# Kernel optimization log

Measured on AMD Instinct MI355X. Metric: run time of the kernel, lower is better.

Reference implementation:

```python
import jax, jax.numpy as jnp
import numpy as np

B, C, H, W = 8, 512, 32, 32
N = H * W
FG_THRES, BG_THRES, TOPK = 0.7, 0.6, 12


def setup_inputs() -> dict:
    key = jax.random.key(0)
    k1, k2, k3 = jax.random.split(key, 3)
    feature_q = jax.random.normal(k1, (B, C, H, W), dtype=jnp.float32)
    support_feat = jax.random.normal(k2, (B, C, H, W), dtype=jnp.float32)
    support_mask = jax.random.randint(k3, (B, H, W), 0, 2).astype(jnp.int32)
    return {"feature_q": feature_q, "support_feat": support_feat, "support_mask": support_mask}


def _masked_avg_pool(feat, mask):
    # feat [B,C,H,W], mask [B,1,H,W]; interpolate to same size is identity
    return jnp.sum(feat * mask, axis=(2, 3)) / (jnp.sum(mask, axis=(2, 3)) + 1e-5)


def _cosine(a, b):
    # F.cosine_similarity along channel dim 1 (eps=1e-8), with broadcasting
    dot = jnp.sum(a * b, axis=1)
    na = jnp.sqrt(jnp.sum(a * a, axis=1))
    nb = jnp.sqrt(jnp.sum(b * b, axis=1))
    return dot / jnp.maximum(na * nb, 1e-8)


def _similarity(feature_q, fg_proto, bg_proto):
    sim_fg = _cosine(feature_q, fg_proto)
    sim_bg = _cosine(feature_q, bg_proto)
    return jnp.stack([sim_bg, sim_fg], axis=1) * 10.0  # [B,2,H,W]


def _select_weights(pred, thres):
    # pred [N] -> float {0,1} selection weights; threshold mask, topk-12 fallback
    m = pred > thres
    _, top_idx = jax.lax.top_k(pred, TOPK)
    tm = jnp.zeros_like(m).at[top_idx].set(True)
    return jnp.where(m.sum() > 0, m, tm).astype(pred.dtype)


def _ssp_single(cur_feat, pred_fg, pred_bg):
    # cur_feat [C,N]; masked formulation == torch's variable-length column select
    wf = _select_weights(pred_fg, FG_THRES)
    wb = _select_weights(pred_bg, BG_THRES)
    fg_proto = jnp.sum(cur_feat * wf, axis=-1) / wf.sum()  # [C]
    bg_proto = jnp.sum(cur_feat * wb, axis=-1) / wb.sum()
    cn = cur_feat / jnp.sqrt(jnp.sum(cur_feat * cur_feat, axis=0, keepdims=True))
    sim = (cn.T @ cn) * 2.0  # [N,N] cosine sim, scaled
    neg = jnp.asarray(-1e30, sim.dtype)
    fg_attn = jax.nn.softmax(jnp.where(wf[None, :] > 0, sim, neg), axis=-1)
    bg_attn = jax.nn.softmax(jnp.where(wb[None, :] > 0, sim, neg), axis=-1)
    fg_local = (fg_attn @ cur_feat.T).T  # [C,N]
    bg_local = (bg_attn @ cur_feat.T).T
    return fg_proto, bg_proto, fg_local, bg_local


def reference(feature_q, support_feat, support_mask):
    mask_f = (support_mask == 1).astype(feature_q.dtype)[:, None]  # [B,1,H,W]
    mask_b = (support_mask == 0).astype(feature_q.dtype)[:, None]
    FP = _masked_avg_pool(support_feat, mask_f)[:, :, None, None]  # [B,C,1,1]
    BP = _masked_avg_pool(support_feat, mask_b)[:, :, None, None]
    out_0 = _similarity(feature_q, FP, BP)  # [B,2,H,W]
    pred = jax.nn.softmax(out_0, axis=1).reshape(B, 2, N)
    cur = feature_q.reshape(B, C, N)
    fg_p, bg_p, fg_l, bg_l = jax.vmap(_ssp_single)(cur, pred[:, 1], pred[:, 0])
    SSFP = fg_p[:, :, None, None]
    SSBP = bg_p[:, :, None, None]
    ASBP = bg_l.reshape(B, C, H, W)
    FP_1 = FP * 0.5 + SSFP * 0.5
    BP_1 = SSBP * 0.3 + ASBP * 0.7
    out_1 = _similarity(feature_q, FP_1, BP_1)  # [B,2,H,W]
    return out_1
```

## Files before the change

### kernel.cpp

```cpp
#include <hip/hip_runtime.h>
#include <math.h>

#define Bsz 8
#define Cch 512
#define Npx 1024
#define TOPK 12
#define BN (Bsz * Npx)

typedef __attribute__((ext_vector_type(8))) short bf16x8;
typedef __attribute__((ext_vector_type(4))) float f32x4;

__device__ __forceinline__ unsigned short f2bf(float x) {
    unsigned u = __float_as_uint(x);
    u += 0x7FFF + ((u >> 16) & 1);
    return (unsigned short)(u >> 16);
}
__device__ __forceinline__ float bf2f(unsigned short h) {
    return __uint_as_float(((unsigned)h) << 16);
}

__device__ __forceinline__ float warp_sum64(float v) {
    for (int o = 32; o > 0; o >>= 1) v += __shfl_down(v, o);
    return v;
}
__device__ __forceinline__ float block_sum512(float v, float* s8) {
    v = warp_sum64(v);
    int lane = threadIdx.x & 63, w = threadIdx.x >> 6;
    __syncthreads();
    if (lane == 0) s8[w] = v;
    __syncthreads();
    float r = 0.f;
    #pragma unroll
    for (int k = 0; k < 8; k++) r += s8[k];
    return r;
}

__global__ void k_pool(const float* __restrict__ sf, const int* __restrict__ mask,
                       float* __restrict__ FPo, float* __restrict__ BPo) {
    __shared__ float s4a[4], s4b[4], s4c[4];
    int c = blockIdx.x, b = blockIdx.y, t = threadIdx.x;
    const float4* f4 = (const float4*)(sf + ((size_t)b * Cch + c) * Npx);
    const int4* m4 = (const int4*)(mask + (size_t)b * Npx);
    float4 v = f4[t];
    int4 m = m4[t];
    float sumf = (m.x == 1 ? v.x : 0.f) + (m.y == 1 ? v.y : 0.f)
               + (m.z == 1 ? v.z : 0.f) + (m.w == 1 ? v.w : 0.f);
    float tot = v.x + v.y + v.z + v.w;
    float cf = (float)((m.x == 1) + (m.y == 1) + (m.z == 1) + (m.w == 1));
    sumf = warp_sum64(sumf);
    tot  = warp_sum64(tot);
    cf   = warp_sum64(cf);
    int lane = t & 63, w = t >> 6;
    if (lane == 0) { s4a[w] = sumf; s4b[w] = tot; s4c[w] = cf; }
    __syncthreads();
    if (t == 0) {
        float sA = s4a[0] + s4a[1] + s4a[2] + s4a[3];
        float sB = s4b[0] + s4b[1] + s4b[2] + s4b[3];
        float sC = s4c[0] + s4c[1] + s4c[2] + s4c[3];
        FPo[b * Cch + c] = sA / (sC + 1e-5f);
        BPo[b * Cch + c] = (sB - sA) / ((1024.f - sC) + 1e-5f);
    }
}

__global__ void __launch_bounds__(512) k_predcast(const float* __restrict__ fq,
                       const float* __restrict__ FP, const float* __restrict__ BP,
                       float* __restrict__ dsim, float* __restrict__ invn,
                       unsigned short* __restrict__ Ft, float* __restrict__ accs) {
    __shared__ float sFP[Cch], sBP[Cch], s8[8];
    __shared__ float rdf[16][32], rdb[16][32], rqq[16][32];
    __shared__ unsigned short S[32][522];
    int b = blockIdx.y, t = threadIdx.x;
    int tx = t & 31, ty = t >> 5;
    int p0 = blockIdx.x * 32;
    int p = p0 + tx;
    if (t < 128) accs[(size_t)(t >> 5) * BN + b * Npx + p0 + (t & 31)] = 0.f;
    sFP[t] = FP[b * Cch + t];
    sBP[t] = BP[b * Cch + t];
    __syncthreads();
    float nf = sqrtf(block_sum512(sFP[t] * sFP[t], s8));
    float nb = sqrtf(block_sum512(sBP[t] * sBP[t], s8));
    const float* q = fq + (size_t)b * Cch * Npx + p;
    float df = 0.f, db = 0.f, qq = 0.f;
    int c0 = ty * 32;
    #pragma unroll 4
    for (int c = 0; c < 32; c += 2) {
        float v0 = q[(size_t)(c0 + c) * Npx];
        float v1 = q[(size_t)(c0 + c + 1) * Npx];
        df += v0 * sFP[c0 + c] + v1 * sFP[c0 + c + 1];
        db += v0 * sBP[c0 + c] + v1 * sBP[c0 + c + 1];
        qq += v0 * v0 + v1 * v1;
        unsigned pk = (unsigned)f2bf(v0) | ((unsigned)f2bf(v1) << 16);
        *(unsigned*)&S[tx][c0 + c] = pk;
    }
    rdf[ty][tx] = df; rdb[ty][tx] = db; rqq[ty][tx] = qq;
    __syncthreads();
    for (int s = 8; s > 0; s >>= 1) {
        if (ty < s) {
            rdf[ty][tx] += rdf[ty + s][tx];
            rdb[ty][tx] += rdb[ty + s][tx];
            rqq[ty][tx] += rqq[ty + s][tx];
        }
        __syncthreads();
    }
    if (ty == 0) {
        float nq = sqrtf(rqq[0][tx]);
        float simf = 10.f * rdf[0][tx] / fmaxf(nq * nf, 1e-8f);
        float simb = 10.f * rdb[0][tx] / fmaxf(nq * nb, 1e-8f);
        dsim[b * Npx + p] = simf - simb;
        invn[b * Npx + p] = 1.f / nq;
    }
    int w = t >> 6, lane = t & 63;
    unsigned short* FtB = Ft + (size_t)b * Npx * Cch;
    for (int pr = w; pr < 32; pr += 8) {
        unsigned* dst = (unsigned*)(FtB + (size_t)(p0 + pr) * Cch);
        #pragma unroll
        for (int it = 0; it < 4; it++) {
            int d = it * 64 + lane;
            dst[d] = *(const unsigned*)&S[pr][d * 2];
        }
    }
}

__global__ void __launch_bounds__(1024) k_selcompact(const float* __restrict__ dsim,
                        const float* __restrict__ invn,
                        const unsigned short* __restrict__ Ft,
                        const float* __restrict__ FP,
                        int* __restrict__ nsf, int* __restrict__ nsb,
                        int* __restrict__ jf, int* __restrict__ jb,
                        float* __restrict__ ivg,
                        float* __restrict__ fgp, float* __restrict__ bgp,
                        float* __restrict__ FP1, float* __restrict__ nfv) {
    __shared__ int wsum[16];
    __shared__ int sns;
    __shared__ float sProto[16][512];
    __shared__ float s16f[16];
    int b = blockIdx.y, t = threadIdx.x;
    int lane = t & 63, w = t >> 6;
    bool isf = (blockIdx.x == 0);
    float d = dsim[b * Npx + t];
    float key = isf ? d : -d;
    float thres = isf ? 0.8472979f : 0.4054651f;
    int flag = (key > thres) ? 1 : 0;
    int x = flag;
    #pragma unroll
    for (int o = 1; o < 64; o <<= 1) {
        int y = __shfl_up(x, o);
        if (lane >= o) x += y;
    }
    if (lane == 63) wsum[w] = x;
    __syncthreads();
    int base = 0, total = 0;
    #pragma unroll
    for (int k = 0; k < 16; k++) {
        int s = wsum[k];
        if (k < w) base += s;
        total += s;
    }
    int* jdst = (isf ? jf : jb) + b * Npx;
    if (total == 0) {
        __shared__ int   sc[Npx];
        __shared__ float v[Npx];
        __shared__ float rv[Npx];
        __shared__ int   ri[Npx];
        v[t] = key; flag = 0;
        __syncthreads();
        for (int k = 0; k < TOPK; k++) {
            rv[t] = v[t]; ri[t] = t;
            __syncthreads();
            for (int s = 512; s > 0; s >>= 1) {
                if (t < s) {
                    float a = rv[t], bb = rv[t + s];
                    int ia = ri[t], ib = ri[t + s];
                    if (bb > a || (bb == a && ib < ia)) { rv[t] = bb; ri[t] = ib; }
                }
                __syncthreads();
            }
            int win = ri[0];
            if (t == win) { flag = 1; v[t] = -INFINITY; }
            __syncthreads();
        }
        sc[t] = flag;
        __syncthreads();
        for (int off = 1; off < 1024; off <<= 1) {
            int xx = (t >= off) ? sc[t - off] : 0;
            __syncthreads();
            sc[t] += xx;
            __syncthreads();
        }
        if (flag) {
            int pos = sc[t] - 1;
            jdst[pos] = t;
            if (!isf) ivg[b * Npx + pos] = invn[b * Npx + t];
        }
        if (t == 1023) sns = sc[1023];
    } else {
        if (flag) {
            int pos = base + x - 1;
            jdst[pos] = t;
            if (!isf) ivg[b * Npx + pos] = invn[b * Npx + t];
        }
        if (t == 0) sns = total;
    }
    __syncthreads();
    int ns = sns;
    if (t == 0) (isf ? nsf : nsb)[b] = ns;
    const unsigned short* FtB = Ft + (size_t)b * Npx * Cch;
    float facc[8] = {0.f, 0.f, 0.f, 0.f, 0.f, 0.f, 0.f, 0.f};
    int k = w;
    int row = (k < ns) ? jdst[k] : 0;
    while (k < ns) {
        int kn = k + 16;
        int rown = (kn < ns) ? jdst[kn] : 0;
        bf16x8 vv = *(const bf16x8*)&FtB[(size_t)row * Cch + lane * 8];
        #pragma unroll
        for (int e = 0; e < 8; e++) facc[e] += bf2f((unsigned short)vv[e]);
        k = kn; row = rown;
    }
    #pragma unroll
    for (int e = 0; e < 8; e++) sProto[w][lane * 8 + e] = facc[e];
    __syncthreads();
    float fp1 = 0.f;
    if (t < 512) {
        float s = 0.f;
        #pragma unroll
        for (int q = 0; q < 16; q++) s += sProto[q][t];
        float pv = s / (float)ns;
        (isf ? fgp : bgp)[b * Cch + t] = pv;
        if (isf) {
            fp1 = 0.5f * FP[b * Cch + t] + 0.5f * pv;
            FP1[b * Cch + t] = fp1;
        }
    }
    if (isf) {
        float v2 = warp_sum64(fp1 * fp1);
        if (lane == 0) s16f[w] = v2;
        __syncthreads();
        if (t == 0) {
            float nn = 0.f;
            #pragma unroll
            for (int q = 0; q < 16; q++) nn += s16f[q];
            nfv[b] = sqrtf(nn);
        }
    }
}

__global__ void __launch_bounds__(256) k_gram_fused(const unsigned short* __restrict__ Ft,
                        const int* __restrict__ jb, const int* __restrict__ nsb,
                        const float* __restrict__ invn, const float* __restrict__ ivg,
                        unsigned short* __restrict__ G, unsigned short* __restrict__ Fg) {
    int b = blockIdx.z;
    int ns = nsb[b];
    int KC = (ns + 31) & ~31;
    if (blockIdx.y >= 16) {
        int j0 = blockIdx.x * 64;
        if (j0 >= KC) return;
        int c0 = (blockIdx.y - 16) * 32;
        __shared__ unsigned short tt[64][34];
        const unsigned short* S = Ft + (size_t)b * Npx * Cch;
        const int* ji = jb + b * Npx;
        int col = threadIdx.x & 31, rr = threadIdx.x >> 5;
        for (int r = rr; r < 64; r += 8) {
            int j = j0 + r;
            int src = (j < ns) ? ji[j] : ji[0];
            tt[r][col] = S[(size_t)src * Cch + c0 + col];
        }
        __syncthreads();
        unsigned* D32 = (unsigned*)(Fg + (size_t)b * Cch * Npx);
        int jx = threadIdx.x & 31;
        for (int cr = rr; cr < 32; cr += 8) {
            unsigned lo = tt[2 * jx][cr], hi = tt[2 * jx + 1][cr];
            D32[(size_t)(c0 + cr) * (Npx / 2) + (j0 >> 1) + jx] = lo | (hi << 16);
        }
        return;
    }
    int j0 = blockIdx.y * 64;
    if (j0 >= KC) return;
    int i0 = blockIdx.x * 64;
    __shared__ unsigned short At[64][72];
    __shared__ unsigned short Bt[64][72];
    __shared__ int sji[64];
    __shared__ float sfi[64], sfj[64];
    const unsigned short* FA = Ft + (size_t)b * Npx * Cch;
    int tid = threadIdx.x;
    if (tid < 64) {
        int j = j0 + tid;
        sji[tid] = (j < ns) ? jb[b * Npx + j] : jb[b * Npx];
        sfj[tid] = (j < ns) ? ivg[b * Npx + j] : 0.f;
        sfi[tid] = 2.f * invn[b * Npx + i0 + tid];
    }
    __syncthreads();
    int rA = tid >> 2, kc8 = (tid & 3) * 8;
    const unsigned short* sa = FA + (size_t)(i0 + rA) * Cch + kc8;
    const unsigned short* sb = FA + (size_t)sji[rA] * Cch + kc8;
    int l = tid & 63, w = tid >> 6;
    int ml = l & 15, quad = l >> 4;
    f32x4 acc[4] = {};
    uint4 a0 = *(const uint4*)sa,        a1 = *(const uint4*)(sa + 32);
    uint4 b0 = *(const uint4*)sb,        b1 = *(const uint4*)(sb + 32);
    for (int k0 = 0; k0 < Cch; k0 += 64) {
        __syncthreads();
        *(uint4*)&At[rA][kc8] = a0;  *(uint4*)&At[rA][kc8 + 32] = a1;
        *(uint4*)&Bt[rA][kc8] = b0;  *(uint4*)&Bt[rA][kc8 + 32] = b1;
        __syncthreads();
        int kn = k0 + 64;
        if (kn < Cch) {
            a0 = *(const uint4*)(sa + kn);  a1 = *(const uint4*)(sa + kn + 32);
            b0 = *(const uint4*)(sb + kn);  b1 = *(const uint4*)(sb + kn + 32);
        }
        #pragma unroll
        for (int h = 0; h < 2; h++) {
            bf16x8 af = *(const bf16x8*)&At[w * 16 + ml][quad * 8 + h * 32];
            bf16x8 bfr[4];
            #pragma unroll
            for (int v = 0; v < 4; v++) bfr[v] = *(const bf16x8*)&Bt[v * 16 + ml][quad * 8 + h * 32];
            #pragma unroll
            for (int v = 0; v < 4; v++)
                acc[v] = __builtin_amdgcn_mfma_f32_16x16x32_bf16(af, bfr[v], acc[v], 0, 0, 0);
        }
    }
    unsigned short* g = G + (size_t)b * Npx * Npx;
    #pragma unroll
    for (int r = 0; r < 4; r++) {
        int il = w * 16 + quad * 4 + r;
        float fi = sfi[il];
        #pragma unroll
        for (int v = 0; v < 4; v++) {
            int jl = v * 16 + ml;
            float e = 0.f;
            if (j0 + jl < ns) e = __expf(acc[v][r] * fi * sfj[jl]);
            g[(size_t)(i0 + il) * Npx + j0 + jl] = f2bf(e);
        }
    }
}

__global__ void __launch_bounds__(256) k_pv_c(const unsigned short* __restrict__ Fg,
                                              const unsigned short* __restrict__ A,
                                              const unsigned short* __restrict__ Ft,
                                              const int* __restrict__ nsb,
                                              const float* __restrict__ bgp,
                                              const float* __restrict__ FP1,
                                              float* __restrict__ accs) {
    int b = blockIdx.z;
    int KC64 = ((((nsb[b] + 31) & ~31) + 63) & ~63);
    __shared__ unsigned short At[64][72];
    __shared__ unsigned short Bt[64][72];
    __shared__ float sfp1[64], sbg[64], sden[64];
    __shared__ float spdb[64], spnb[64], spdf[64], spqq[64];
    int i0 = blockIdx.x * 64, c0 = blockIdx.y * 64;
    const unsigned short* F = Fg + (size_t)b * Cch * Npx;
    const unsigned short* Ar = A + (size_t)b * Npx * Npx;
    int tid = threadIdx.x;
    if (tid < 64) {
        sfp1[tid] = FP1[b * Cch + c0 + tid];
        sbg[tid] = 0.3f * bgp[b * Cch + c0 + tid];
    }
    int rr = tid >> 2, kc8 = (tid & 3) * 8;
    const unsigned short* sa = F + (size_t)(c0 + rr) * Npx + kc8;
    const unsigned short* sb = Ar + (size_t)(i0 + rr) * Npx + kc8;
    int l = tid & 63, w = tid >> 6;
    int ml = l & 15, quad = l >> 4;
    f32x4 acc[4] = {};
    float dsum = 0.f;
    uint4 a0 = *(const uint4*)sa,  a1 = *(const uint4*)(sa + 32);
    uint4 b0 = *(const uint4*)sb,  b1 = *(const uint4*)(sb + 32);
    for (int j0 = 0; j0 < KC64; j0 += 64) {
        __syncthreads();
        *(uint4*)&At[rr][kc8] = a0;  *(uint4*)&At[rr][kc8 + 32] = a1;
        *(uint4*)&Bt[rr][kc8] = b0;  *(uint4*)&Bt[rr][kc8 + 32] = b1;
        dsum += __uint_as_float(b0.x << 16) + __uint_as_float(b0.x & 0xFFFF0000u)
              + __uint_as_float(b0.y << 16) + __uint_as_float(b0.y & 0xFFFF0000u)
              + __uint_as_float(b0.z << 16) + __uint_as_float(b0.z & 0xFFFF0000u)
              + __uint_as_float(b0.w << 16) + __uint_as_float(b0.w & 0xFFFF0000u)
              + __uint_as_float(b1.x << 16) + __uint_as_float(b1.x & 0xFFFF0000u)
              + __uint_as_float(b1.y << 16) + __uint_as_float(b1.y & 0xFFFF0000u)
              + __uint_as_float(b1.z << 16) + __uint_as_float(b1.z & 0xFFFF0000u)
              + __uint_as_float(b1.w << 16) + __uint_as_float(b1.w & 0xFFFF0000u);
        __syncthreads();
        int jn = j0 + 64;
        if (jn < KC64) {
            a0 = *(const uint4*)(sa + jn);  a1 = *(const uint4*)(sa + jn + 32);
            b0 = *(const uint4*)(sb + jn);  b1 = *(const uint4*)(sb + jn + 32);
        }
        #pragma unroll
        for (int h = 0; h < 2; h++) {
            bf16x8 af = *(const bf16x8*)&At[w * 16 + ml][quad * 8 + h * 32];
            bf16x8 bfr[4];
            #pragma unroll
            for (int v = 0; v < 4; v++) bfr[v] = *(const bf16x8*)&Bt[v * 16 + ml][quad * 8 + h * 32];
            #pragma unroll
            for (int v = 0; v < 4; v++)
                acc[v] = __builtin_amdgcn_mfma_f32_16x16x32_bf16(af, bfr[v], acc[v], 0, 0, 0);
        }
    }
    dsum += __shfl_xor(dsum, 1);
    dsum += __shfl_xor(dsum, 2);
    if ((tid & 3) == 0) sden[rr] = dsum;
    __syncthreads();
    {
        const unsigned short* src = Ft + (size_t)b * Npx * Cch + (size_t)(i0 + (tid >> 2)) * Cch + c0 + (tid & 3) * 16;
        *(uint4*)&At[tid >> 2][(tid & 3) * 16] = *(const uint4*)src;
        *(uint4*)&At[tid >> 2][(tid & 3) * 16 + 8] = *(const uint4*)(src + 8);
    }
    if (tid < 64) { spdb[tid] = 0.f; spnb[tid] = 0.f; spdf[tid] = 0.f; spqq[tid] = 0.f; }
    float rd[4];
    #pragma unroll
    for (int v = 0; v < 4; v++) rd[v] = 1.f / sden[v * 16 + ml];
    __syncthreads();
    #pragma unroll
    for (int v = 0; v < 4; v++) {
        int iloc = v * 16 + ml;
        float sdb = 0.f, snb = 0.f, sdf = 0.f, sqq = 0.f;
        #pragma unroll
        for (int r = 0; r < 4; r++) {
            int cl = w * 16 + quad * 4 + r;
            float loc = acc[v][r] * rd[v];
            float bp1 = sbg[cl] + 0.7f * loc;
            float qv = bf2f(At[iloc][cl]);
            sdb += qv * bp1;
            snb += bp1 * bp1;
            sdf += qv * sfp1[cl];
            sqq += qv * qv;
        }
        #pragma unroll
        for (int m = 16; m < 64; m <<= 1) {
            sdb += __shfl_xor(sdb, m);
            snb += __shfl_xor(snb, m);
            sdf += __shfl_xor(sdf, m);
            sqq += __shfl_xor(sqq, m);
        }
        if (quad == 0) {
            atomicAdd(&spdb[iloc], sdb);
            atomicAdd(&spnb[iloc], snb);
            atomicAdd(&spdf[iloc], sdf);
            atomicAdd(&spqq[iloc], sqq);
        }
    }
    __syncthreads();
    {
        int a = tid >> 6, idx = tid & 63;
        float v = (a == 0) ? spdb[idx] : (a == 1) ? spnb[idx] : (a == 2) ? spdf[idx] : spqq[idx];
        atomicAdd(&accs[(size_t)a * BN + b * Npx + i0 + idx], v);
    }
}

__global__ void k_fin(const float* __restrict__ accs, const float* __restrict__ nfv,
                      float* __restrict__ out) {
    int b = blockIdx.y;
    int p = blockIdx.x * 256 + threadIdx.x;
    int base = b * Npx + p;
    float db = accs[(size_t)0 * BN + base];
    float nb = accs[(size_t)1 * BN + base];
    float df = accs[(size_t)2 * BN + base];
    float qq = accs[(size_t)3 * BN + base];
    float nq = sqrtf(qq);
    float sf = 10.f * df / fmaxf(nq * nfv[b], 1e-8f);
    float sb = 10.f * db / fmaxf(nq * sqrtf(nb), 1e-8f);
    out[((size_t)b * 2) * Npx + p] = sb;
    out[((size_t)b * 2 + 1) * Npx + p] = sf;
}

extern "C" void kernel_launch(void* const* d_in, const int* in_sizes, int n_in,
                              void* d_out, int out_size, void* d_ws, size_t ws_size,
                              hipStream_t stream) {
    const float* fq = (const float*)d_in[0];
    const float* sf = (const float*)d_in[1];
    const int* mask = (const int*)d_in[2];
    float* out = (float*)d_out;

    float* ws = (float*)d_ws;
    float* FP    = ws;
    float* BP    = FP + Bsz * Cch;
    float* fgp   = BP + Bsz * Cch;
    float* bgp   = fgp + Bsz * Cch;
    float* FP1   = bgp + Bsz * Cch;
    float* nfv   = FP1 + Bsz * Cch;
    float* dsim  = nfv + 8;
    float* invn  = dsim + BN;
    float* ivg   = invn + BN;
    int*   nsf   = (int*)(ivg + BN);
    int*   nsb   = nsf + 8;
    int*   jf    = nsb + 8;
    int*   jb    = jf + BN;
    float* accs  = (float*)(jb + BN);
    unsigned short* Ft = (unsigned short*)(accs + (size_t)4 * BN);
    unsigned short* Fg = Ft + (size_t)Bsz * Npx * Cch;
    unsigned short* Gb = Fg + (size_t)Bsz * Cch * Npx;

    k_pool<<<dim3(Cch, Bsz), 256, 0, stream>>>(sf, mask, FP, BP);
    k_predcast<<<dim3(Npx / 32, Bsz), 512, 0, stream>>>(fq, FP, BP, dsim, invn, Ft, accs);
    k_selcompact<<<dim3(2, Bsz), 1024, 0, stream>>>(dsim, invn, Ft, FP, nsf, nsb, jf, jb, ivg, fgp, bgp, FP1, nfv);
    k_gram_fused<<<dim3(16, 32, Bsz), 256, 0, stream>>>(Ft, jb, nsb, invn, ivg, Gb, Fg);
    k_pv_c<<<dim3(Npx / 64, Cch / 64, Bsz), 256, 0, stream>>>(Fg, Gb, Ft, nsb, bgp, FP1, accs);
    k_fin<<<dim3(Npx / 256, Bsz), 256, 0, stream>>>(accs, nfv, out);
}
```

Before: 132.7 us.

## Fuse gram, attention-value and finalize into one flash-style kernel

Replaces the separate gram (exp-similarity written to global bf16), PV GEMM and finalize kernels with a single kernel per 32-row query tile. That kernel keeps the query rows and the exp-similarity row block in shared memory, computes the denominator and attention-weighted features, and writes the final cosine scores directly. This removes the global G and Fg buffers, the accumulator zeroing and the global atomics. In exchange it launches only 256 blocks with heavy shared-memory use (about 100KB), which lowers occupancy and parallelism. It also redoes the gathered-feature loads for each query tile.

```diff
diff --git a/kernel.cpp b/kernel.cpp
--- a/kernel.cpp
+++ b/kernel.cpp
@@ -65,7 +65,7 @@
 __global__ void __launch_bounds__(512) k_predcast(const float* __restrict__ fq,
                        const float* __restrict__ FP, const float* __restrict__ BP,
                        float* __restrict__ dsim, float* __restrict__ invn,
-                       unsigned short* __restrict__ Ft, float* __restrict__ accs) {
+                       unsigned short* __restrict__ Ft) {
     __shared__ float sFP[Cch], sBP[Cch], s8[8];
     __shared__ float rdf[16][32], rdb[16][32], rqq[16][32];
     __shared__ unsigned short S[32][522];
@@ -73,7 +73,6 @@
     int tx = t & 31, ty = t >> 5;
     int p0 = blockIdx.x * 32;
     int p = p0 + tx;
-    if (t < 128) accs[(size_t)(t >> 5) * BN + b * Npx + p0 + (t & 31)] = 0.f;
     sFP[t] = FP[b * Cch + t];
     sBP[t] = BP[b * Cch + t];
     __syncthreads();
@@ -244,219 +243,153 @@
     }
 }
 
-__global__ void __launch_bounds__(256) k_gram_fused(const unsigned short* __restrict__ Ft,
-                        const int* __restrict__ jb, const int* __restrict__ nsb,
-                        const float* __restrict__ invn, const float* __restrict__ ivg,
-                        unsigned short* __restrict__ G, unsigned short* __restrict__ Fg) {
-    int b = blockIdx.z;
-    int ns = nsb[b];
-    int KC = (ns + 31) & ~31;
-    if (blockIdx.y >= 16) {
-        int j0 = blockIdx.x * 64;
-        if (j0 >= KC) return;
-        int c0 = (blockIdx.y - 16) * 32;
-        __shared__ unsigned short tt[64][34];
-        const unsigned short* S = Ft + (size_t)b * Npx * Cch;
-        const int* ji = jb + b * Npx;
-        int col = threadIdx.x & 31, rr = threadIdx.x >> 5;
-        for (int r = rr; r < 64; r += 8) {
-            int j = j0 + r;
-            int src = (j < ns) ? ji[j] : ji[0];
-            tt[r][col] = S[(size_t)src * Cch + c0 + col];
-        }
-        __syncthreads();
-        unsigned* D32 = (unsigned*)(Fg + (size_t)b * Cch * Npx);
-        int jx = threadIdx.x & 31;
-        for (int cr = rr; cr < 32; cr += 8) {
-            unsigned lo = tt[2 * jx][cr], hi = tt[2 * jx + 1][cr];
-            D32[(size_t)(c0 + cr) * (Npx / 2) + (j0 >> 1) + jx] = lo | (hi << 16);
-        }
-        return;
-    }
-    int j0 = blockIdx.y * 64;
-    if (j0 >= KC) return;
-    int i0 = blockIdx.x * 64;
-    __shared__ unsigned short At[64][72];
-    __shared__ unsigned short Bt[64][72];
-    __shared__ int sji[64];
-    __shared__ float sfi[64], sfj[64];
-    const unsigned short* FA = Ft + (size_t)b * Npx * Cch;
+__global__ void __launch_bounds__(512) k_fused(
+        const unsigned short* __restrict__ Ft,
+        const int* __restrict__ jb, const int* __restrict__ nsb,
+        const float* __restrict__ invn, const float* __restrict__ ivg,
+        const float* __restrict__ bgp, const float* __restrict__ FP1,
+        const float* __restrict__ nfv, float* __restrict__ out) {
+    __shared__ unsigned short Afull[32][520];
+    __shared__ unsigned short sP[32][1032];
+    __shared__ unsigned short Bt[64][136];
+    __shared__ int   sji[1024];
+    __shared__ float sfj[1024];
+    __shared__ float sfi[32], sden[32];
+    __shared__ float sfp1c[64], sbgc[64];
+    __shared__ float spart[32][4];
+
+    int b = blockIdx.y;
+    int i0 = blockIdx.x * 32;
     int tid = threadIdx.x;
-    if (tid < 64) {
-        int j = j0 + tid;
-        sji[tid] = (j < ns) ? jb[b * Npx + j] : jb[b * Npx];
-        sfj[tid] = (j < ns) ? ivg[b * Npx + j] : 0.f;
-        sfi[tid] = 2.f * invn[b * Npx + i0 + tid];
-    }
-    __syncthreads();
-    int rA = tid >> 2, kc8 = (tid & 3) * 8;
-    const unsigned short* sa = FA + (size_t)(i0 + rA) * Cch + kc8;
-    const unsigned short* sb = FA + (size_t)sji[rA] * Cch + kc8;
     int l = tid & 63, w = tid >> 6;
     int ml = l & 15, quad = l >> 4;
-    f32x4 acc[4] = {};
-    uint4 a0 = *(const uint4*)sa,        a1 = *(const uint4*)(sa + 32);
-    uint4 b0 = *(const uint4*)sb,        b1 = *(const uint4*)(sb + 32);
-    for (int k0 = 0; k0 < Cch; k0 += 64) {
+    int ns = nsb[b];
+    int K64 = ((((ns + 31) & ~31) + 63) & ~63);
+
+    const unsigned short* FtB = Ft + (size_t)b * Npx * Cch;
+
+    #pragma unroll
+    for (int s = 0; s < 4; s++) {
+        int idx = tid + s * 512;
+        int row = idx >> 6, kc8 = (idx & 63) * 8;
+        *(uint4*)&Afull[row][kc8] = *(const uint4*)(FtB + (size_t)(i0 + row) * Cch + kc8);
+    }
+    for (int j = tid; j < K64; j += 512) {
+        sji[j] = (j < ns) ? jb[b * Npx + j] : jb[b * Npx];
+        sfj[j] = (j < ns) ? ivg[b * Npx + j] : 0.f;
+    }
+    if (tid < 32) sfi[tid] = 2.f * invn[b * Npx + i0 + tid];
+    __syncthreads();
+
+    int ig = w & 1, jg = w >> 1;
+    for (int j0 = 0; j0 < K64; j0 += 64) {
+        const unsigned short* pb0 = FtB + (size_t)sji[j0 + (tid >> 4)] * Cch + (tid & 15) * 8;
+        const unsigned short* pb1 = FtB + (size_t)sji[j0 + 32 + (tid >> 4)] * Cch + (tid & 15) * 8;
+        uint4 v0 = *(const uint4*)pb0;
+        uint4 v1 = *(const uint4*)pb1;
+        f32x4 acc = {};
+        for (int k0 = 0; k0 < Cch; k0 += 128) {
+            __syncthreads();
+            *(uint4*)&Bt[tid >> 4][(tid & 15) * 8] = v0;
+            *(uint4*)&Bt[32 + (tid >> 4)][(tid & 15) * 8] = v1;
+            __syncthreads();
+            int kn = k0 + 128;
+            if (kn < Cch) {
+                v0 = *(const uint4*)(pb0 + kn);
+                v1 = *(const uint4*)(pb1 + kn);
+            }
+            #pragma unroll
+            for (int h = 0; h < 4; h++) {
+                bf16x8 af = *(const bf16x8*)&Afull[ig * 16 + ml][k0 + h * 32 + quad * 8];
+                bf16x8 bf = *(const bf16x8*)&Bt[jg * 16 + ml][h * 32 + quad * 8];
+                acc = __builtin_amdgcn_mfma_f32_16x16x32_bf16(af, bf, acc, 0, 0, 0);
+            }
+        }
+        #pragma unroll
+        for (int r = 0; r < 4; r++) {
+            int il = ig * 16 + quad * 4 + r;
+            int jl = jg * 16 + ml;
+            float e = (j0 + jl < ns) ? __expf(acc[r] * sfi[il] * sfj[j0 + jl]) : 0.f;
+            sP[il][j0 + jl] = f2bf(e);
+        }
+    }
+    __syncthreads();
+
+    {
+        int i = tid >> 4, jj16 = tid & 15;
+        float s = 0.f;
+        for (int j = jj16; j < K64; j += 16) s += bf2f(sP[i][j]);
+        #pragma unroll
+        for (int m = 1; m < 16; m <<= 1) s += __shfl_xor(s, m);
+        if (jj16 == 0) sden[i] = s;
+    }
+    if (tid < 128) ((float*)spart)[tid] = 0.f;
+    __syncthreads();
+
+    int cgw = w & 3, igw = w >> 2;
+    int icol = igw * 16 + ml;
+    float rdi = 1.f / sden[icol];
+    float sdb = 0.f, snb = 0.f, sdf = 0.f, sqq = 0.f;
+    int jj = tid & 63, cg = tid >> 6;
+    for (int c0 = 0; c0 < Cch; c0 += 64) {
         __syncthreads();
-        *(uint4*)&At[rA][kc8] = a0;  *(uint4*)&At[rA][kc8 + 32] = a1;
-        *(uint4*)&Bt[rA][kc8] = b0;  *(uint4*)&Bt[rA][kc8 + 32] = b1;
-        __syncthreads();
-        int kn = k0 + 64;
-        if (kn < Cch) {
-            a0 = *(const uint4*)(sa + kn);  a1 = *(const uint4*)(sa + kn + 32);
-            b0 = *(const uint4*)(sb + kn);  b1 = *(const uint4*)(sb + kn + 32);
-        }
-        #pragma unroll
-        for (int h = 0; h < 2; h++) {
-            bf16x8 af = *(const bf16x8*)&At[w * 16 + ml][quad * 8 + h * 32];
-            bf16x8 bfr[4];
+        if (tid < 64) {
+            sfp1c[tid] = FP1[b * Cch + c0 + tid];
+            sbgc[tid]  = 0.3f * bgp[b * Cch + c0 + tid];
+        }
+        f32x4 accp = {};
+        uint4 vv = *(const uint4*)(FtB + (size_t)sji[jj] * Cch + c0 + cg * 8);
+        for (int j0 = 0; j0 < K64; j0 += 64) {
+            __syncthreads();
+            {
+                unsigned short* qd = &Bt[cg * 8][jj];
+                qd[0]       = (unsigned short)vv.x;  qd[136]     = (unsigned short)(vv.x >> 16);
+                qd[2 * 136] = (unsigned short)vv.y;  qd[3 * 136] = (unsigned short)(vv.y >> 16);
+                qd[4 * 136] = (unsigned short)vv.z;  qd[5 * 136] = (unsigned short)(vv.z >> 16);
+                qd[6 * 136] = (unsigned short)vv.w;  qd[7 * 136] = (unsigned short)(vv.w >> 16);
+            }
+            __syncthreads();
+            int jn = j0 + 64;
+            if (jn < K64) vv = *(const uint4*)(FtB + (size_t)sji[jn + jj] * Cch + c0 + cg * 8);
             #pragma unroll
-            for (int v = 0; v < 4; v++) bfr[v] = *(const bf16x8*)&Bt[v * 16 + ml][quad * 8 + h * 32];
-            #pragma unroll
-            for (int v = 0; v < 4; v++)
-                acc[v] = __builtin_amdgcn_mfma_f32_16x16x32_bf16(af, bfr[v], acc[v], 0, 0, 0);
-        }
-    }
-    unsigned short* g = G + (size_t)b * Npx * Npx;
-    #pragma unroll
-    for (int r = 0; r < 4; r++) {
-        int il = w * 16 + quad * 4 + r;
-        float fi = sfi[il];
-        #pragma unroll
-        for (int v = 0; v < 4; v++) {
-            int jl = v * 16 + ml;
-            float e = 0.f;
-            if (j0 + jl < ns) e = __expf(acc[v][r] * fi * sfj[jl]);
-            g[(size_t)(i0 + il) * Npx + j0 + jl] = f2bf(e);
-        }
-    }
-}
-
-__global__ void __launch_bounds__(256) k_pv_c(const unsigned short* __restrict__ Fg,
-                                              const unsigned short* __restrict__ A,
-                                              const unsigned short* __restrict__ Ft,
-                                              const int* __restrict__ nsb,
-                                              const float* __restrict__ bgp,
-                                              const float* __restrict__ FP1,
-                                              float* __restrict__ accs) {
-    int b = blockIdx.z;
-    int KC64 = ((((nsb[b] + 31) & ~31) + 63) & ~63);
-    __shared__ unsigned short At[64][72];
-    __shared__ unsigned short Bt[64][72];
-    __shared__ float sfp1[64], sbg[64], sden[64];
-    __shared__ float spdb[64], spnb[64], spdf[64], spqq[64];
-    int i0 = blockIdx.x * 64, c0 = blockIdx.y * 64;
-    const unsigned short* F = Fg + (size_t)b * Cch * Npx;
-    const unsigned short* Ar = A + (size_t)b * Npx * Npx;
-    int tid = threadIdx.x;
-    if (tid < 64) {
-        sfp1[tid] = FP1[b * Cch + c0 + tid];
-        sbg[tid] = 0.3f * bgp[b * Cch + c0 + tid];
-    }
-    int rr = tid >> 2, kc8 = (tid & 3) * 8;
-    const unsigned short* sa = F + (size_t)(c0 + rr) * Npx + kc8;
-    const unsigned short* sb = Ar + (size_t)(i0 + rr) * Npx + kc8;
-    int l = tid & 63, w = tid >> 6;
-    int ml = l & 15, quad = l >> 4;
-    f32x4 acc[4] = {};
-    float dsum = 0.f;
-    uint4 a0 = *(const uint4*)sa,  a1 = *(const uint4*)(sa + 32);
-    uint4 b0 = *(const uint4*)sb,  b1 = *(const uint4*)(sb + 32);
-    for (int j0 = 0; j0 < KC64; j0 += 64) {
-        __syncthreads();
-        *(uint4*)&At[rr][kc8] = a0;  *(uint4*)&At[rr][kc8 + 32] = a1;
-        *(uint4*)&Bt[rr][kc8] = b0;  *(uint4*)&Bt[rr][kc8 + 32] = b1;
-        dsum += __uint_as_float(b0.x << 16) + __uint_as_float(b0.x & 0xFFFF0000u)
-              + __uint_as_float(b0.y << 16) + __uint_as_float(b0.y & 0xFFFF0000u)
-              + __uint_as_float(b0.z << 16) + __uint_as_float(b0.z & 0xFFFF0000u)
-              + __uint_as_float(b0.w << 16) + __uint_as_float(b0.w & 0xFFFF0000u)
-              + __uint_as_float(b1.x << 16) + __uint_as_float(b1.x & 0xFFFF0000u)
-              + __uint_as_float(b1.y << 16) + __uint_as_float(b1.y & 0xFFFF0000u)
-              + __uint_as_float(b1.z << 16) + __uint_as_float(b1.z & 0xFFFF0000u)
-              + __uint_as_float(b1.w << 16) + __uint_as_float(b1.w & 0xFFFF0000u);
-        __syncthreads();
-        int jn = j0 + 64;
-        if (jn < KC64) {
-            a0 = *(const uint4*)(sa + jn);  a1 = *(const uint4*)(sa + jn + 32);
-            b0 = *(const uint4*)(sb + jn);  b1 = *(const uint4*)(sb + jn + 32);
-        }
-        #pragma unroll
-        for (int h = 0; h < 2; h++) {
-            bf16x8 af = *(const bf16x8*)&At[w * 16 + ml][quad * 8 + h * 32];
-            bf16x8 bfr[4];
-            #pragma unroll
-            for (int v = 0; v < 4; v++) bfr[v] = *(const bf16x8*)&Bt[v * 16 + ml][quad * 8 + h * 32];
-            #pragma unroll
-            for (int v = 0; v < 4; v++)
-                acc[v] = __builtin_amdgcn_mfma_f32_16x16x32_bf16(af, bfr[v], acc[v], 0, 0, 0);
-        }
-    }
-    dsum += __shfl_xor(dsum, 1);
-    dsum += __shfl_xor(dsum, 2);
-    if ((tid & 3) == 0) sden[rr] = dsum;
-    __syncthreads();
-    {
-        const unsigned short* src = Ft + (size_t)b * Npx * Cch + (size_t)(i0 + (tid >> 2)) * Cch + c0 + (tid & 3) * 16;
-        *(uint4*)&At[tid >> 2][(tid & 3) * 16] = *(const uint4*)src;
-        *(uint4*)&At[tid >> 2][(tid & 3) * 16 + 8] = *(const uint4*)(src + 8);
-    }
-    if (tid < 64) { spdb[tid] = 0.f; spnb[tid] = 0.f; spdf[tid] = 0.f; spqq[tid] = 0.f; }
-    float rd[4];
-    #pragma unroll
-    for (int v = 0; v < 4; v++) rd[v] = 1.f / sden[v * 16 + ml];
-    __syncthreads();
-    #pragma unroll
-    for (int v = 0; v < 4; v++) {
-        int iloc = v * 16 + ml;
-        float sdb = 0.f, snb = 0.f, sdf = 0.f, sqq = 0.f;
+            for (int hh = 0; hh < 2; hh++) {
+                bf16x8 af  = *(const bf16x8*)&Bt[cgw * 16 + ml][hh * 32 + quad * 8];
+                bf16x8 bfr = *(const bf16x8*)&sP[icol][j0 + hh * 32 + quad * 8];
+                accp = __builtin_amdgcn_mfma_f32_16x16x32_bf16(af, bfr, accp, 0, 0, 0);
+            }
+        }
         #pragma unroll
         for (int r = 0; r < 4; r++) {
-            int cl = w * 16 + quad * 4 + r;
-            float loc = acc[v][r] * rd[v];
-            float bp1 = sbg[cl] + 0.7f * loc;
-            float qv = bf2f(At[iloc][cl]);
+            int cl = cgw * 16 + quad * 4 + r;
+            float loc = accp[r] * rdi;
+            float bp1 = sbgc[cl] + 0.7f * loc;
+            float qv = bf2f(Afull[icol][c0 + cl]);
             sdb += qv * bp1;
             snb += bp1 * bp1;
-            sdf += qv * sfp1[cl];
+            sdf += qv * sfp1c[cl];
             sqq += qv * qv;
         }
-        #pragma unroll
-        for (int m = 16; m < 64; m <<= 1) {
-            sdb += __shfl_xor(sdb, m);
-            snb += __shfl_xor(snb, m);
-            sdf += __shfl_xor(sdf, m);
-            sqq += __shfl_xor(sqq, m);
-        }
-        if (quad == 0) {
-            atomicAdd(&spdb[iloc], sdb);
-            atomicAdd(&spnb[iloc], snb);
-            atomicAdd(&spdf[iloc], sdf);
-            atomicAdd(&spqq[iloc], sqq);
-        }
-    }
-    __syncthreads();
-    {
-        int a = tid >> 6, idx = tid & 63;
-        float v = (a == 0) ? spdb[idx] : (a == 1) ? spnb[idx] : (a == 2) ? spdf[idx] : spqq[idx];
-        atomicAdd(&accs[(size_t)a * BN + b * Npx + i0 + idx], v);
-    }
-}
-
-__global__ void k_fin(const float* __restrict__ accs, const float* __restrict__ nfv,
-                      float* __restrict__ out) {
-    int b = blockIdx.y;
-    int p = blockIdx.x * 256 + threadIdx.x;
-    int base = b * Npx + p;
-    float db = accs[(size_t)0 * BN + base];
-    float nb = accs[(size_t)1 * BN + base];
-    float df = accs[(size_t)2 * BN + base];
-    float qq = accs[(size_t)3 * BN + base];
-    float nq = sqrtf(qq);
-    float sf = 10.f * df / fmaxf(nq * nfv[b], 1e-8f);
-    float sb = 10.f * db / fmaxf(nq * sqrtf(nb), 1e-8f);
-    out[((size_t)b * 2) * Npx + p] = sb;
-    out[((size_t)b * 2 + 1) * Npx + p] = sf;
+    }
+    sdb += __shfl_xor(sdb, 16);  sdb += __shfl_xor(sdb, 32);
+    snb += __shfl_xor(snb, 16);  snb += __shfl_xor(snb, 32);
+    sdf += __shfl_xor(sdf, 16);  sdf += __shfl_xor(sdf, 32);
+    sqq += __shfl_xor(sqq, 16);  sqq += __shfl_xor(sqq, 32);
+    if (quad == 0) {
+        atomicAdd(&spart[icol][0], sdb);
+        atomicAdd(&spart[icol][1], snb);
+        atomicAdd(&spart[icol][2], sdf);
+        atomicAdd(&spart[icol][3], sqq);
+    }
+    __syncthreads();
+    if (tid < 32) {
+        float db = spart[tid][0], nb = spart[tid][1];
+        float df = spart[tid][2], qq = spart[tid][3];
+        float nq = sqrtf(qq);
+        float sb2 = 10.f * db / fmaxf(nq * sqrtf(nb), 1e-8f);
+        float sf2 = 10.f * df / fmaxf(nq * nfv[b], 1e-8f);
+        out[((size_t)b * 2) * Npx + i0 + tid] = sb2;
+        out[((size_t)b * 2 + 1) * Npx + i0 + tid] = sf2;
+    }
 }
 
 extern "C" void kernel_launch(void* const* d_in, const int* in_sizes, int n_in,
@@ -481,15 +414,10 @@
     int*   nsb   = nsf + 8;
     int*   jf    = nsb + 8;
     int*   jb    = jf + BN;
-    float* accs  = (float*)(jb + BN);
-    unsigned short* Ft = (unsigned short*)(accs + (size_t)4 * BN);
-    unsigned short* Fg = Ft + (size_t)Bsz * Npx * Cch;
-    unsigned short* Gb = Fg + (size_t)Bsz * Cch * Npx;
+    unsigned short* Ft = (unsigned short*)(jb + BN);
 
     k_pool<<<dim3(Cch, Bsz), 256, 0, stream>>>(sf, mask, FP, BP);
-    k_predcast<<<dim3(Npx / 32, Bsz), 512, 0, stream>>>(fq, FP, BP, dsim, invn, Ft, accs);
+    k_predcast<<<dim3(Npx / 32, Bsz), 512, 0, stream>>>(fq, FP, BP, dsim, invn, Ft);
     k_selcompact<<<dim3(2, Bsz), 1024, 0, stream>>>(dsim, invn, Ft, FP, nsf, nsb, jf, jb, ivg, fgp, bgp, FP1, nfv);
-    k_gram_fused<<<dim3(16, 32, Bsz), 256, 0, stream>>>(Ft, jb, nsb, invn, ivg, Gb, Fg);
-    k_pv_c<<<dim3(Npx / 64, Cch / 64, Bsz), 256, 0, stream>>>(Fg, Gb, Ft, nsb, bgp, FP1, accs);
-    k_fin<<<dim3(Npx / 256, Bsz), 256, 0, stream>>>(accs, nfv, out);
-}
+    k_fused<<<dim3(32, Bsz), 512, 0, stream>>>(Ft, jb, nsb, invn, ivg, bgp, FP1, nfv, out);
+}
```

Result: no change. 130.6 us (-1.6%).
